# Performance work log

Hardware: AMD Instinct MI355X
Metric: run time of the kernel (lower is better)

The kernel has to match this reference:

```python
import jax, jax.numpy as jnp
import numpy as np

B = 8192; N_LEAF = 34; N_SUB = 11; D0 = 32; ES = 64; EA = 128; H = 4
ETH = slice(0, 8); IP = slice(8, 19); TCP = slice(19, 34)
TCPF = slice(0, 8); IPF = slice(8, 11)


def setup_inputs() -> dict:
    key = jax.random.key(0)
    ks = jax.random.split(key, 32)
    w = lambda i, s: jax.random.normal(ks[i], s, dtype=jnp.float32) * 0.05
    return {
        "leaf_feats": jax.random.normal(ks[0], (B, N_LEAF, D0), dtype=jnp.float32),
        "sub_feats": jax.random.normal(ks[1], (B, N_SUB, D0), dtype=jnp.float32),
        "sub_align_W": w(2, (N_SUB, D0, ES)), "sub_align_b": w(3, (N_SUB, ES)),
        "leaf_align_W": w(4, (N_LEAF, D0, EA)), "leaf_align_b": w(5, (N_LEAF, EA)),
        "parent_align_W": w(6, (2, ES, EA)), "parent_align_b": w(7, (2, EA)),
        "sA_cls": w(8, (2, ES)), "sA_Wqkv": w(9, (2, 3 * ES, ES)), "sA_bqkv": w(10, (2, 3 * ES)),
        "sA_Wo": w(11, (2, ES, ES)), "sA_bo": w(12, (2, ES)),
        "sA_lng": jnp.ones((2, ES), jnp.float32), "sA_lnb": jnp.zeros((2, ES), jnp.float32),
        "sA_W1": w(13, (2, ES, 4 * ES)), "sA_b1": w(14, (2, 4 * ES)),
        "sA_W2": w(15, (2, 4 * ES, ES)), "sA_b2": w(16, (2, ES)),
        "pA_cls": w(17, (4, EA)), "pA_Wqkv": w(18, (4, 3 * EA, EA)), "pA_bqkv": w(19, (4, 3 * EA)),
        "pA_Wo": w(20, (4, EA, EA)), "pA_bo": w(21, (4, EA)),
        "pA_lng": jnp.ones((4, EA), jnp.float32), "pA_lnb": jnp.zeros((4, EA), jnp.float32),
        "pA_W1": w(22, (4, EA, 4 * EA)), "pA_b1": w(23, (4, 4 * EA)),
        "pA_W2": w(24, (4, 4 * EA, EA)), "pA_b2": w(25, (4, EA)),
        "clf_W": w(26, (EA, 2)), "clf_b": w(27, (2,)),
    }


def _ln(t, g, b):
    m = jnp.mean(t, -1, keepdims=True)
    v = jnp.var(t, -1, keepdims=True)
    return (t - m) / jnp.sqrt(v + 1e-5) * g + b


def _agg(x, cls, Wqkv, bqkv, Wo, bo, lng, lnb, W1, b1, W2, b2):
    # AttentionAggregator: prepend CLS, MHA, shared LayerNorm twice, FFN; return CLS output.
    Bx, _, E = x.shape
    d = E // H
    xc = jnp.concatenate([jnp.broadcast_to(cls, (Bx, 1, E)), x], axis=1)  # [B,S,E]
    S = xc.shape[1]
    qkv = xc @ Wqkv.T + bqkv                      # torch MHA in_proj layout [3E,E]
    q, k, v = jnp.split(qkv, 3, axis=-1)
    sh = lambda t: t.reshape(Bx, S, H, d).transpose(0, 2, 1, 3)
    q, k, v = sh(q), sh(k), sh(v)
    a = jax.nn.softmax(jnp.einsum('bhqd,bhkd->bhqk', q, k) * (1.0 / np.sqrt(d)), axis=-1)
    o = jnp.einsum('bhqk,bhkd->bhqd', a, v).transpose(0, 2, 1, 3).reshape(Bx, S, E)
    o = o @ Wo.T + bo
    h = _ln(xc + o, lng, lnb)
    f = jax.nn.gelu(h @ W1 + b1, approximate=False) @ W2 + b2
    h = _ln(h + f, lng, lnb)
    return h[:, 0]


def reference(leaf_feats, sub_feats, sub_align_W, sub_align_b, leaf_align_W, leaf_align_b,
              parent_align_W, parent_align_b,
              sA_cls, sA_Wqkv, sA_bqkv, sA_Wo, sA_bo, sA_lng, sA_lnb, sA_W1, sA_b1, sA_W2, sA_b2,
              pA_cls, pA_Wqkv, pA_bqkv, pA_Wo, pA_bo, pA_lng, pA_lnb, pA_W1, pA_b1, pA_W2, pA_b2,
              clf_W, clf_b):
    sA = lambda i: (sA_cls[i], sA_Wqkv[i], sA_bqkv[i], sA_Wo[i], sA_bo[i], sA_lng[i], sA_lnb[i],
                    sA_W1[i], sA_b1[i], sA_W2[i], sA_b2[i])
    pA = lambda i: (pA_cls[i], pA_Wqkv[i], pA_bqkv[i], pA_Wo[i], pA_bo[i], pA_lng[i], pA_lnb[i],
                    pA_W1[i], pA_b1[i], pA_W2[i], pA_b2[i])
    # subfield align (per-subfield Linear, batched) + aggregate
    sub_al = jnp.einsum('bsd,sde->bse', sub_feats, sub_align_W) + sub_align_b  # [B,11,64]
    tcpf = _agg(sub_al[:, TCPF], *sA(0))   # tcp.flags -> [B,64]
    ipf = _agg(sub_al[:, IPF], *sA(1))     # ip.flags  -> [B,64]
    # per-field aligners to aligned_dim=128
    leaf_al = jnp.einsum('bfd,fde->bfe', leaf_feats, leaf_align_W) + leaf_align_b  # [B,34,128]
    parent_al = jnp.stack([tcpf @ parent_align_W[0] + parent_align_b[0],
                           ipf @ parent_align_W[1] + parent_align_b[1]], axis=1)   # [B,2,128]
    eth_vec = _agg(leaf_al[:, ETH], *pA(0))
    ip_vec = _agg(jnp.concatenate([leaf_al[:, IP], parent_al[:, 1:2]], axis=1), *pA(1))
    tcp_vec = _agg(jnp.concatenate([leaf_al[:, TCP], parent_al[:, 0:1]], axis=1), *pA(2))
    pkt = _agg(jnp.stack([eth_vec, ip_vec, tcp_vec], axis=1), *pA(3))
    return pkt @ clf_W + clf_b
```

## Files before the change

### kernel.cpp

```cpp
#include <hip/hip_runtime.h>
#include <math.h>

#define G 4
#define NT 256


enum {
  I_LEAF = 0, I_SUB, I_SAW, I_SAB, I_LAW, I_LAB, I_PAW, I_PAB,
  I_SCLS, I_SWQKV, I_SBQKV, I_SWO, I_SBO, I_SLNG, I_SLNB, I_SW1, I_SB1, I_SW2, I_SB2,
  I_PCLS, I_PWQKV, I_PBQKV, I_PWO, I_PBO, I_PLNG, I_PLNB, I_PW1, I_PB1, I_PW2, I_PB2,
  I_CLFW, I_CLFB
};

struct P {
  const float* in[32];
  float* parent_al;
  float* vecs;
  float* out;
};

__device__ float g_usb[6][520];

__device__ __forceinline__ void LD8(const float* p, float* o) {
  float4 a = ((const float4*)p)[0], b = ((const float4*)p)[1];
  o[0] = a.x; o[1] = a.y; o[2] = a.z; o[3] = a.w;
  o[4] = b.x; o[5] = b.y; o[6] = b.z; o[7] = b.w;
}
__device__ __forceinline__ void fma8(float& acc, const float* x, const float* w) {
#pragma unroll
  for (int i = 0; i < 8; ++i) acc += x[i] * w[i];
}
__device__ __forceinline__ float gelu(float v) {
  return 0.5f * v * (1.0f + erff(v * 0.70710678118654752f));
}

template <int E>
__device__ void ln_rows(float* buf, const float* __restrict__ gg, const float* __restrict__ bb) {
  const int w = threadIdx.x >> 6, lane = threadIdx.x & 63;
  for (int g = w; g < G; g += 4) {
    float* row = buf + g * E;
    float s = 0.f, s2 = 0.f;
    for (int e = lane; e < E; e += 64) { float x = row[e]; s += x; s2 += x * x; }
#pragma unroll
    for (int off = 1; off < 64; off <<= 1) {
      s += __shfl_xor(s, off, 64);
      s2 += __shfl_xor(s2, off, 64);
    }
    float m = s / (float)E;
    float inv = 1.0f / sqrtf(s2 / (float)E - m * m + 1e-5f);
    for (int e = lane; e < E; e += 64) row[e] = (row[e] - m) * inv * gg[e] + bb[e];
  }
}

__global__ __launch_bounds__(NT) void k_setup(P p) {
  const int a = blockIdx.x;
  const int tid = threadIdx.x;
  __shared__ float clsb[128];
  __shared__ float qb[128];
  int E;
  const float *Wq, *bq, *cls;
  if (a < 2) {
    E = 64;
    Wq = p.in[I_SWQKV] + (size_t)a * 192 * 64;
    bq = p.in[I_SBQKV] + a * 192;
    cls = p.in[I_SCLS] + a * 64;
  } else {
    E = 128;
    int i = a - 2;
    Wq = p.in[I_PWQKV] + (size_t)i * 384 * 128;
    bq = p.in[I_PBQKV] + i * 384;
    cls = p.in[I_PCLS] + i * 128;
  }
  const int D = E / 4;
  const float scale = (E == 64) ? 0.25f : 0.17677669529663687f;
  if (tid < E) clsb[tid] = cls[tid];
  __syncthreads();
  if (tid < E) {
    float acc = bq[tid];
    const float* w = Wq + (size_t)tid * E;
    for (int k = 0; k < E; k += 8) {
      float wv[8];
      LD8(w + k, wv);
#pragma unroll
      for (int ii = 0; ii < 8; ++ii) acc += clsb[k + ii] * wv[ii];
    }
    qb[tid] = acc;
  }
  __syncthreads();
  if (tid < E) {
    for (int h = 0; h < 4; ++h) {
      float acc = 0.f;
      for (int d = 0; d < D; ++d)
        acc += Wq[(size_t)(E + h * D + d) * E + tid] * qb[h * D + d];
      g_usb[a][h * E + tid] = acc * scale;
    }
  }
  if (tid < 4) {
    float acc = 0.f;
    for (int d = 0; d < D; ++d) acc += qb[tid * D + d] * bq[E + tid * D + d];
    g_usb[a][4 * E + tid] = acc * scale;
  }
}

template <int E, int T, int XP>
__device__ void agg_run(const float* X, const float* clsb,
                        const float* uL, const float* sbL,
                        const float* __restrict__ Wv, const float* __restrict__ bv,
                        const float* __restrict__ Wo, const float* __restrict__ bo,
                        const float* __restrict__ lng, const float* __restrict__ lnb,
                        const float* __restrict__ W1, const float* __restrict__ b1,
                        const float* __restrict__ W2, const float* __restrict__ b2,
                        float* att, float* xbar, float* ob, float* hb, float* mid,
                        float* partial) {
  const int tid = threadIdx.x;
  constexpr int S = T + 1, KS = NT / E, KCH = E / KS;
  constexpr int M1 = (4 * E) / NT, KCH2 = (4 * E) / KS;

  for (int i = tid; i < G * 4 * S; i += NT) {
    int s = i % S, hh = (i / S) % 4, g = i / (4 * S);
    const float* u = uL + hh * XP;
    const float* x = (s == 0) ? clsb : (X + (size_t)(g * T + s - 1) * XP);
    float acc = sbL[hh];
    for (int k = 0; k < E; k += 8) {
      float xv[8], uv[8];
      LD8(x + k, xv);
      LD8(u + k, uv);
      fma8(acc, xv, uv);
    }
    att[(g * 4 + hh) * S + s] = acc;
  }
  __syncthreads();
  for (int i = tid; i < G * 4; i += NT) {
    float* a = att + i * S;
    float mx = a[0];
    for (int s = 1; s < S; ++s) mx = fmaxf(mx, a[s]);
    float sum = 0.f;
    for (int s = 0; s < S; ++s) { float e = expf(a[s] - mx); a[s] = e; sum += e; }
    float inv = 1.0f / sum;
    for (int s = 0; s < S; ++s) a[s] *= inv;
  }
  __syncthreads();
  constexpr int NI = (G * 4 * E) / NT;
  float xacc[NI];
#pragma unroll
  for (int n = 0; n < NI; ++n) {
    int i = tid + n * NT;
    int k = i % E, hh = (i / E) % 4, g = i / (4 * E);
    const float* a = att + (g * 4 + hh) * S;
    float acc = a[0] * clsb[k];
    for (int s = 1; s < S; ++s) acc += a[s] * X[(size_t)(g * T + s - 1) * XP + k];
    xacc[n] = acc;
  }
  __syncthreads();
#pragma unroll
  for (int n = 0; n < NI; ++n) xbar[tid + n * NT] = xacc[n];
  __syncthreads();
  {
    const int e = tid % E, ks = tid / E, hh = e / (E / 4);
    const float* w = Wv + (size_t)e * E + ks * KCH;
    float acc[G];
#pragma unroll
    for (int g = 0; g < G; ++g) acc[g] = 0.f;
    for (int kc = 0; kc < KCH; kc += 8) {
      float wv[8];
      LD8(w + kc, wv);
#pragma unroll
      for (int g = 0; g < G; ++g) {
        float xv[8];
        LD8(xbar + (g * 4 + hh) * E + ks * KCH + kc, xv);
        fma8(acc[g], xv, wv);
      }
    }
#pragma unroll
    for (int g = 0; g < G; ++g) partial[(ks * G + g) * E + e] = acc[g];
  }
  __syncthreads();
  for (int i = tid; i < G * E; i += NT) {
    int e = i % E, g = i / E;
    float v = bv[e];
#pragma unroll
    for (int ks = 0; ks < KS; ++ks) v += partial[(ks * G + g) * E + e];
    ob[g * E + e] = v;
  }
  __syncthreads();
  {
    const int e = tid % E, ks = tid / E;
    const float* w = Wo + (size_t)e * E + ks * KCH;
    float acc[G];
#pragma unroll
    for (int g = 0; g < G; ++g) acc[g] = 0.f;
    for (int kc = 0; kc < KCH; kc += 8) {
      float wv[8];
      LD8(w + kc, wv);
#pragma unroll
      for (int g = 0; g < G; ++g) {
        float xv[8];
        LD8(ob + g * E + ks * KCH + kc, xv);
        fma8(acc[g], xv, wv);
      }
    }
#pragma unroll
    for (int g = 0; g < G; ++g) partial[(ks * G + g) * E + e] = acc[g];
  }
  __syncthreads();
  for (int i = tid; i < G * E; i += NT) {
    int e = i % E, g = i / E;
    float v = bo[e] + clsb[e];
#pragma unroll
    for (int ks = 0; ks < KS; ++ks) v += partial[(ks * G + g) * E + e];
    hb[g * E + e] = v;
  }
  __syncthreads();
  ln_rows<E>(hb, lng, lnb);
  __syncthreads();
  {
    float acc[M1][G];
#pragma unroll
    for (int r = 0; r < M1; ++r)
#pragma unroll
      for (int g = 0; g < G; ++g) acc[r][g] = 0.f;
    for (int j = 0; j < E; j += 8) {
      float wv[M1][8];
#pragma unroll
      for (int ii = 0; ii < 8; ++ii) {
        if constexpr (M1 == 2) {
          float2 w2 = *(const float2*)(W1 + (size_t)(j + ii) * 4 * E + 2 * tid);
          wv[0][ii] = w2.x;
          wv[1][ii] = w2.y;
        } else {
          wv[0][ii] = W1[(size_t)(j + ii) * 4 * E + tid];
        }
      }
#pragma unroll
      for (int g = 0; g < G; ++g) {
        float xv[8];
        LD8(hb + g * E + j, xv);
#pragma unroll
        for (int r = 0; r < M1; ++r) fma8(acc[r][g], xv, wv[r]);
      }
    }
#pragma unroll
    for (int r = 0; r < M1; ++r) {
      int m = tid * M1 + r;
      float bias = b1[m];
#pragma unroll
      for (int g = 0; g < G; ++g) mid[g * 4 * E + m] = gelu(acc[r][g] + bias);
    }
  }
  __syncthreads();
  {
    const int e = tid % E, ks = tid / E, m0 = ks * KCH2;
    float acc[G];
#pragma unroll
    for (int g = 0; g < G; ++g) acc[g] = 0.f;
    for (int mc = 0; mc < KCH2; mc += 8) {
      float wv[8];
#pragma unroll
      for (int ii = 0; ii < 8; ++ii) wv[ii] = W2[(size_t)(m0 + mc + ii) * E + e];
#pragma unroll
      for (int g = 0; g < G; ++g) {
        float xv[8];
        LD8(mid + g * 4 * E + m0 + mc, xv);
        fma8(acc[g], xv, wv);
      }
    }
#pragma unroll
    for (int g = 0; g < G; ++g) partial[(ks * G + g) * E + e] = acc[g];
  }
  __syncthreads();
  for (int i = tid; i < G * E; i += NT) {
    int e = i % E, g = i / E;
    float v = b2[e] + hb[g * E + e];
#pragma unroll
    for (int ks = 0; ks < KS; ++ks) v += partial[(ks * G + g) * E + e];
    ob[g * E + e] = v;
  }
  __syncthreads();
  ln_rows<E>(ob, lng, lnb);
  __syncthreads();
}

__global__ __launch_bounds__(NT, 4) void k_sub(P p) {
  constexpr int XP = 68;
  __shared__ __align__(16) float X1[G * 8 * XP];
  __shared__ __align__(16) float X2[G * 3 * XP];
  __shared__ __align__(16) float clsb[64];
  __shared__ __align__(16) float uL[4 * XP];
  __shared__ __align__(16) float sbL[4];
  __shared__ __align__(16) float att[G * 4 * 9];
  __shared__ __align__(16) float xbar[G * 4 * 64];
  __shared__ __align__(16) float ob[G * 64];
  __shared__ __align__(16) float hb[G * 64];
  __shared__ __align__(16) float mid[G * 256];
  __shared__ __align__(16) float partial[4 * G * 64];
  __shared__ __align__(16) float vec1[G * 64];
  const int tid = threadIdx.x, b0 = blockIdx.x * G;

  const float* subf = p.in[I_SUB];
  const float* saW = p.in[I_SAW];
  const float* sab = p.in[I_SAB];
  for (int i = tid; i < 11 * 64; i += NT) {
    int f = i / 64, e = i % 64;
    float bias = sab[f * 64 + e];
    float acc[G];
#pragma unroll
    for (int g = 0; g < G; ++g) acc[g] = bias;
    for (int d = 0; d < 32; d += 8) {
      float wv[8];
#pragma unroll
      for (int ii = 0; ii < 8; ++ii) wv[ii] = saW[(size_t)(f * 32 + d + ii) * 64 + e];
#pragma unroll
      for (int g = 0; g < G; ++g) {
        float xv[8];
        LD8(subf + (size_t)(b0 + g) * 352 + f * 32 + d, xv);
        fma8(acc[g], xv, wv);
      }
    }
#pragma unroll
    for (int g = 0; g < G; ++g) {
      if (f < 8) X1[(g * 8 + f) * XP + e] = acc[g];
      else       X2[(g * 3 + f - 8) * XP + e] = acc[g];
    }
  }
  for (int i = tid; i < 4 * 64; i += NT) uL[(i >> 6) * XP + (i & 63)] = g_usb[0][i];
  if (tid < 4) sbL[tid] = g_usb[0][256 + tid];
  if (tid < 64) clsb[tid] = p.in[I_SCLS][tid];
  __syncthreads();

  agg_run<64, 8, XP>(X1, clsb, uL, sbL,
                     p.in[I_SWQKV] + 2 * 64 * 64, p.in[I_SBQKV] + 128,
                     p.in[I_SWO], p.in[I_SBO], p.in[I_SLNG], p.in[I_SLNB],
                     p.in[I_SW1], p.in[I_SB1], p.in[I_SW2], p.in[I_SB2],
                     att, xbar, ob, hb, mid, partial);
  for (int i = tid; i < G * 64; i += NT) vec1[i] = ob[i];

  for (int i = tid; i < 4 * 64; i += NT) uL[(i >> 6) * XP + (i & 63)] = g_usb[1][i];
  if (tid < 4) sbL[tid] = g_usb[1][256 + tid];
  if (tid < 64) clsb[tid] = p.in[I_SCLS][64 + tid];
  __syncthreads();

  agg_run<64, 3, XP>(X2, clsb, uL, sbL,
                     p.in[I_SWQKV] + 192 * 64 + 2 * 64 * 64, p.in[I_SBQKV] + 192 + 128,
                     p.in[I_SWO] + 64 * 64, p.in[I_SBO] + 64,
                     p.in[I_SLNG] + 64, p.in[I_SLNB] + 64,
                     p.in[I_SW1] + 64 * 256, p.in[I_SB1] + 256,
                     p.in[I_SW2] + 256 * 64, p.in[I_SB2] + 64,
                     att, xbar, ob, hb, mid, partial);

  {
    const int pi = tid >> 7, e = tid & 127;
    const float* paW = p.in[I_PAW];
    float bias = p.in[I_PAB][pi * 128 + e];
    float acc[G];
#pragma unroll
    for (int g = 0; g < G; ++g) acc[g] = bias;
    const float* src = pi ? ob : vec1;
    for (int j = 0; j < 64; j += 8) {
      float wv[8];
#pragma unroll
      for (int ii = 0; ii < 8; ++ii) wv[ii] = paW[(size_t)(pi * 64 + j + ii) * 128 + e];
#pragma unroll
      for (int g = 0; g < G; ++g) {
        float xv[8];
        LD8(src + g * 64 + j, xv);
        fma8(acc[g], xv, wv);
      }
    }
#pragma unroll
    for (int g = 0; g < G; ++g)
      p.parent_al[(size_t)(b0 + g) * 256 + pi * 128 + e] = acc[g];
  }
}

#define PXP 132
#define OVL 6144

template <int T, int F, int F0, int PAR, int AI>
__device__ void parent_body(const P& p, int b0, float* arena, float* clsb,
                            float* uL, float* sbL, float* att) {
  const int tid = threadIdx.x;
  float* X = arena;
  const float* leaf = p.in[I_LEAF];
  const float* laW = p.in[I_LAW];
  const float* lab = p.in[I_LAB];
  for (int i = tid; i < F * 128; i += NT) {
    int f = i / 128, e = i % 128;
    float bias = lab[(F0 + f) * 128 + e];
    float acc[G];
#pragma unroll
    for (int g = 0; g < G; ++g) acc[g] = bias;
    for (int d = 0; d < 32; d += 8) {
      float wv[8];
#pragma unroll
      for (int ii = 0; ii < 8; ++ii)
        wv[ii] = laW[(size_t)((F0 + f) * 32 + d + ii) * 128 + e];
#pragma unroll
      for (int g = 0; g < G; ++g) {
        float xv[8];
        LD8(leaf + (size_t)(b0 + g) * 1088 + (F0 + f) * 32 + d, xv);
        fma8(acc[g], xv, wv);
      }
    }
#pragma unroll
    for (int g = 0; g < G; ++g) X[(g * T + f) * PXP + e] = acc[g];
  }
  if constexpr (PAR >= 0) {
    for (int i = tid; i < G * 128; i += NT) {
      int g = i / 128, e = i % 128;
      X[(g * T + T - 1) * PXP + e] = p.parent_al[(size_t)(b0 + g) * 256 + PAR * 128 + e];
    }
  }
  for (int i = tid; i < 4 * 128; i += NT) uL[(i >> 7) * PXP + (i & 127)] = g_usb[2 + AI][i];
  if (tid < 4) sbL[tid] = g_usb[2 + AI][512 + tid];
  if (tid < 128) clsb[tid] = p.in[I_PCLS][AI * 128 + tid];
  __syncthreads();

  float* xbar = arena;
  float* partial = arena + 2048;
  float* ob = arena + 3072;
  float* hb = arena + 3584;
  float* mid = arena + 4096;
  agg_run<128, T, PXP>(X, clsb, uL, sbL,
                       p.in[I_PWQKV] + (size_t)AI * 384 * 128 + 2 * 128 * 128,
                       p.in[I_PBQKV] + AI * 384 + 256,
                       p.in[I_PWO] + (size_t)AI * 128 * 128, p.in[I_PBO] + AI * 128,
                       p.in[I_PLNG] + AI * 128, p.in[I_PLNB] + AI * 128,
                       p.in[I_PW1] + (size_t)AI * 128 * 512, p.in[I_PB1] + AI * 512,
                       p.in[I_PW2] + (size_t)AI * 512 * 128, p.in[I_PB2] + AI * 128,
                       att, xbar, ob, hb, mid, partial);
  for (int i = tid; i < G * 128; i += NT) {
    int e = i % 128, g = i / 128;
    p.vecs[(size_t)(b0 + g) * 384 + AI * 128 + e] = ob[g * 128 + e];
  }
}

#define PARENT_KERNEL(NAME, T, F, F0, PAR, AI, ASZ)                         \
__global__ __launch_bounds__(NT, 4) void NAME(P p) {                        \
  __shared__ __align__(16) float arena[ASZ];                                \
  __shared__ __align__(16) float clsb[128];                                 \
  __shared__ __align__(16) float uL[4 * PXP];                               \
  __shared__ __align__(16) float sbL[4];                                    \
  __shared__ __align__(16) float att[G * 4 * (T + 1)];                      \
  parent_body<T, F, F0, PAR, AI>(p, blockIdx.x * G, arena, clsb, uL, sbL, att); \
}

PARENT_KERNEL(k_parent0,  8,  8,  0, -1, 0, OVL)
PARENT_KERNEL(k_parent1, 12, 11,  8,  1, 1, G * 12 * PXP)
PARENT_KERNEL(k_parent2, 16, 15, 19,  0, 2, G * 16 * PXP)

__global__ __launch_bounds__(NT, 4) void k_pkt(P p) {
  __shared__ __align__(16) float arena[OVL];
  __shared__ __align__(16) float clsb[128];
  __shared__ __align__(16) float uL[4 * PXP];
  __shared__ __align__(16) float sbL[4];
  __shared__ __align__(16) float att[G * 4 * 4];
  const int tid = threadIdx.x, b0 = blockIdx.x * G;
  float* X = arena;

  for (int i = tid; i < 3 * G * 128; i += NT) {
    int e = i % 128, g = (i / 128) % G, t = i / (G * 128);
    X[(g * 3 + t) * PXP + e] = p.vecs[(size_t)(b0 + g) * 384 + t * 128 + e];
  }
  for (int i = tid; i < 4 * 128; i += NT) uL[(i >> 7) * PXP + (i & 127)] = g_usb[5][i];
  if (tid < 4) sbL[tid] = g_usb[5][512 + tid];
  if (tid < 128) clsb[tid] = p.in[I_PCLS][3 * 128 + tid];
  __syncthreads();

  float* xbar = arena;
  float* partial = arena + 2048;
  float* ob = arena + 3072;
  float* hb = arena + 3584;
  float* mid = arena + 4096;
  agg_run<128, 3, PXP>(X, clsb, uL, sbL,
                       p.in[I_PWQKV] + (size_t)3 * 384 * 128 + 2 * 128 * 128,
                       p.in[I_PBQKV] + 3 * 384 + 256,
                       p.in[I_PWO] + (size_t)3 * 128 * 128, p.in[I_PBO] + 3 * 128,
                       p.in[I_PLNG] + 3 * 128, p.in[I_PLNB] + 3 * 128,
                       p.in[I_PW1] + (size_t)3 * 128 * 512, p.in[I_PB1] + 3 * 512,
                       p.in[I_PW2] + (size_t)3 * 512 * 128, p.in[I_PB2] + 3 * 128,
                       att, xbar, ob, hb, mid, partial);

  if (tid < G * 2) {
    int g = tid >> 1, c = tid & 1;
    const float* cw = p.in[I_CLFW];
    float acc = p.in[I_CLFB][c];
    for (int j = 0; j < 128; ++j) acc += ob[g * 128 + j] * cw[j * 2 + c];
    p.out[(size_t)(b0 + g) * 2 + c] = acc;
  }
}

extern "C" void kernel_launch(void* const* d_in, const int* in_sizes, int n_in,
                              void* d_out, int out_size, void* d_ws, size_t ws_size,
                              hipStream_t stream) {
  P p;
  for (int i = 0; i < 32; ++i) p.in[i] = (const float*)d_in[i];
  const int B = in_sizes[0] / (34 * 32);
  float* ws = (float*)d_ws;
  p.parent_al = ws;
  p.vecs = ws + (size_t)B * 256;
  p.out = (float*)d_out;

  k_setup<<<dim3(6), dim3(NT), 0, stream>>>(p);
  k_sub<<<dim3(B / G), dim3(NT), 0, stream>>>(p);
  k_parent0<<<dim3(B / G), dim3(NT), 0, stream>>>(p);
  k_parent1<<<dim3(B / G), dim3(NT), 0, stream>>>(p);
  k_parent2<<<dim3(B / G), dim3(NT), 0, stream>>>(p);
  k_pkt<<<dim3(B / G), dim3(NT), 0, stream>>>(p);
}
```

Before: 1.064 ms.

## Split subfield kernel into per-aggregator kernels plus parent-align kernel

Splits the single k_sub kernel into three launches: one per subfield aggregator (tcp.flags, ip.flags) and a separate kernel for the parent-align projection. Intermediate aggregator outputs now go through global memory (vecs) instead of shared memory. The aim is to cut per-block shared memory (only one X buffer per kernel) and specialise each kernel so occupancy rises. In exchange it adds two extra launches and a global round trip for the intermediate vectors.

```diff
diff --git a/kernel.cpp b/kernel.cpp
--- a/kernel.cpp
+++ b/kernel.cpp
@@ -280,96 +280,95 @@
   __syncthreads();
 }
 
-__global__ __launch_bounds__(NT, 4) void k_sub(P p) {
+template <int T, int F0, int AI>
+__device__ void sub_body(const P& p, int b0) {
   constexpr int XP = 68;
-  __shared__ __align__(16) float X1[G * 8 * XP];
-  __shared__ __align__(16) float X2[G * 3 * XP];
+  const int tid = threadIdx.x;
+  __shared__ __align__(16) float X[G * T * XP];
   __shared__ __align__(16) float clsb[64];
   __shared__ __align__(16) float uL[4 * XP];
   __shared__ __align__(16) float sbL[4];
-  __shared__ __align__(16) float att[G * 4 * 9];
+  __shared__ __align__(16) float att[G * 4 * (T + 1)];
   __shared__ __align__(16) float xbar[G * 4 * 64];
   __shared__ __align__(16) float ob[G * 64];
   __shared__ __align__(16) float hb[G * 64];
   __shared__ __align__(16) float mid[G * 256];
   __shared__ __align__(16) float partial[4 * G * 64];
-  __shared__ __align__(16) float vec1[G * 64];
-  const int tid = threadIdx.x, b0 = blockIdx.x * G;
 
   const float* subf = p.in[I_SUB];
   const float* saW = p.in[I_SAW];
   const float* sab = p.in[I_SAB];
-  for (int i = tid; i < 11 * 64; i += NT) {
+  for (int i = tid; i < T * 64; i += NT) {
     int f = i / 64, e = i % 64;
-    float bias = sab[f * 64 + e];
+    float bias = sab[(F0 + f) * 64 + e];
     float acc[G];
 #pragma unroll
     for (int g = 0; g < G; ++g) acc[g] = bias;
     for (int d = 0; d < 32; d += 8) {
       float wv[8];
 #pragma unroll
-      for (int ii = 0; ii < 8; ++ii) wv[ii] = saW[(size_t)(f * 32 + d + ii) * 64 + e];
+      for (int ii = 0; ii < 8; ++ii)
+        wv[ii] = saW[(size_t)((F0 + f) * 32 + d + ii) * 64 + e];
 #pragma unroll
       for (int g = 0; g < G; ++g) {
         float xv[8];
-        LD8(subf + (size_t)(b0 + g) * 352 + f * 32 + d, xv);
+        LD8(subf + (size_t)(b0 + g) * 352 + (F0 + f) * 32 + d, xv);
         fma8(acc[g], xv, wv);
       }
     }
 #pragma unroll
+    for (int g = 0; g < G; ++g) X[(g * T + f) * XP + e] = acc[g];
+  }
+  for (int i = tid; i < 4 * 64; i += NT) uL[(i >> 6) * XP + (i & 63)] = g_usb[AI][i];
+  if (tid < 4) sbL[tid] = g_usb[AI][256 + tid];
+  if (tid < 64) clsb[tid] = p.in[I_SCLS][AI * 64 + tid];
+  __syncthreads();
+
+  agg_run<64, T, XP>(X, clsb, uL, sbL,
+                     p.in[I_SWQKV] + AI * 192 * 64 + 2 * 64 * 64,
+                     p.in[I_SBQKV] + AI * 192 + 128,
+                     p.in[I_SWO] + AI * 64 * 64, p.in[I_SBO] + AI * 64,
+                     p.in[I_SLNG] + AI * 64, p.in[I_SLNB] + AI * 64,
+                     p.in[I_SW1] + AI * 64 * 256, p.in[I_SB1] + AI * 256,
+                     p.in[I_SW2] + AI * 256 * 64, p.in[I_SB2] + AI * 64,
+                     att, xbar, ob, hb, mid, partial);
+  for (int i = tid; i < G * 64; i += NT) {
+    int e = i % 64, g = i / 64;
+    p.vecs[(size_t)(b0 + g) * 384 + AI * 64 + e] = ob[g * 64 + e];
+  }
+}
+
+__global__ __launch_bounds__(NT, 4) void k_sub_agg0(P p) { sub_body<8, 0, 0>(p, blockIdx.x * G); }
+__global__ __launch_bounds__(NT, 4) void k_sub_agg1(P p) { sub_body<3, 8, 1>(p, blockIdx.x * G); }
+
+__global__ __launch_bounds__(NT, 4) void k_pal(P p) {
+  __shared__ __align__(16) float tf[G * 128];
+  const int tid = threadIdx.x, b0 = blockIdx.x * G;
+  for (int i = tid; i < G * 128; i += NT) {
+    int g = i / 128, r = i % 128;
+    tf[i] = p.vecs[(size_t)(b0 + g) * 384 + r];
+  }
+  __syncthreads();
+  const int pi = tid >> 7, e = tid & 127;
+  const float* paW = p.in[I_PAW];
+  float bias = p.in[I_PAB][pi * 128 + e];
+  float acc[G];
+#pragma unroll
+  for (int g = 0; g < G; ++g) acc[g] = bias;
+  for (int j = 0; j < 64; j += 8) {
+    float wv[8];
+#pragma unroll
+    for (int ii = 0; ii < 8; ++ii) wv[ii] = paW[(size_t)(pi * 64 + j + ii) * 128 + e];
+#pragma unroll
     for (int g = 0; g < G; ++g) {
-      if (f < 8) X1[(g * 8 + f) * XP + e] = acc[g];
-      else       X2[(g * 3 + f - 8) * XP + e] = acc[g];
-    }
-  }
-  for (int i = tid; i < 4 * 64; i += NT) uL[(i >> 6) * XP + (i & 63)] = g_usb[0][i];
-  if (tid < 4) sbL[tid] = g_usb[0][256 + tid];
-  if (tid < 64) clsb[tid] = p.in[I_SCLS][tid];
-  __syncthreads();
-
-  agg_run<64, 8, XP>(X1, clsb, uL, sbL,
-                     p.in[I_SWQKV] + 2 * 64 * 64, p.in[I_SBQKV] + 128,
-                     p.in[I_SWO], p.in[I_SBO], p.in[I_SLNG], p.in[I_SLNB],
-                     p.in[I_SW1], p.in[I_SB1], p.in[I_SW2], p.in[I_SB2],
-                     att, xbar, ob, hb, mid, partial);
-  for (int i = tid; i < G * 64; i += NT) vec1[i] = ob[i];
-
-  for (int i = tid; i < 4 * 64; i += NT) uL[(i >> 6) * XP + (i & 63)] = g_usb[1][i];
-  if (tid < 4) sbL[tid] = g_usb[1][256 + tid];
-  if (tid < 64) clsb[tid] = p.in[I_SCLS][64 + tid];
-  __syncthreads();
-
-  agg_run<64, 3, XP>(X2, clsb, uL, sbL,
-                     p.in[I_SWQKV] + 192 * 64 + 2 * 64 * 64, p.in[I_SBQKV] + 192 + 128,
-                     p.in[I_SWO] + 64 * 64, p.in[I_SBO] + 64,
-                     p.in[I_SLNG] + 64, p.in[I_SLNB] + 64,
-                     p.in[I_SW1] + 64 * 256, p.in[I_SB1] + 256,
-                     p.in[I_SW2] + 256 * 64, p.in[I_SB2] + 64,
-                     att, xbar, ob, hb, mid, partial);
-
-  {
-    const int pi = tid >> 7, e = tid & 127;
-    const float* paW = p.in[I_PAW];
-    float bias = p.in[I_PAB][pi * 128 + e];
-    float acc[G];
-#pragma unroll
-    for (int g = 0; g < G; ++g) acc[g] = bias;
-    const float* src = pi ? ob : vec1;
-    for (int j = 0; j < 64; j += 8) {
-      float wv[8];
-#pragma unroll
-      for (int ii = 0; ii < 8; ++ii) wv[ii] = paW[(size_t)(pi * 64 + j + ii) * 128 + e];
-#pragma unroll
-      for (int g = 0; g < G; ++g) {
-        float xv[8];
-        LD8(src + g * 64 + j, xv);
-        fma8(acc[g], xv, wv);
-      }
-    }
-#pragma unroll
-    for (int g = 0; g < G; ++g)
-      p.parent_al[(size_t)(b0 + g) * 256 + pi * 128 + e] = acc[g];
-  }
+      float xv[8];
+      LD8(tf + g * 128 + pi * 64 + j, xv);
+      fma8(acc[g], xv, wv);
+    }
+  }
+#pragma unroll
+  for (int g = 0; g < G; ++g)
+    p.parent_al[(size_t)(b0 + g) * 256 + pi * 128 + e] = acc[g];
 }
 
 #define PXP 132
@@ -501,7 +500,9 @@
   p.out = (float*)d_out;
 
   k_setup<<<dim3(6), dim3(NT), 0, stream>>>(p);
-  k_sub<<<dim3(B / G), dim3(NT), 0, stream>>>(p);
+  k_sub_agg0<<<dim3(B / G), dim3(NT), 0, stream>>>(p);
+  k_sub_agg1<<<dim3(B / G), dim3(NT), 0, stream>>>(p);
+  k_pal<<<dim3(B / G), dim3(NT), 0, stream>>>(p);
   k_parent0<<<dim3(B / G), dim3(NT), 0, stream>>>(p);
   k_parent1<<<dim3(B / G), dim3(NT), 0, stream>>>(p);
   k_parent2<<<dim3(B / G), dim3(NT), 0, stream>>>(p);
```

Result: faster. 996.7 us (-6.3%).
